# Kernel optimization log

Measured on AMD Instinct MI355X. Metric: run time of the kernel, lower is better.

## Reference

```python
import jax, jax.numpy as jnp
import numpy as np

B = 4          # clouds per batch
N_PER = 8192   # points per cloud
RATIO = 0.5
M = int(N_PER * RATIO)   # sampled centroids per cloud
R = 0.2        # radius
K = 64         # max_num_neighbors
C_IN = 64


def setup_inputs() -> dict:
    key = jax.random.key(0)
    k1, k2, k3, k4 = jax.random.split(key, 4)
    N = B * N_PER
    x = jax.random.normal(k1, (N, C_IN), dtype=jnp.float32)
    pos = jax.random.uniform(k2, (N, 3), dtype=jnp.float32)  # unit cube
    batch = jnp.repeat(jnp.arange(B, dtype=jnp.int32), N_PER)
    W1 = jax.random.normal(k3, (C_IN + 3, 64), dtype=jnp.float32) * (1.0 / np.sqrt(C_IN + 3))
    b1 = jnp.zeros((64,), dtype=jnp.float32)
    W2 = jax.random.normal(k4, (64, 128), dtype=jnp.float32) * (1.0 / np.sqrt(64))
    b2 = jnp.zeros((128,), dtype=jnp.float32)
    return {"x": x, "pos": pos, "batch": batch, "W1": W1, "b1": b1, "W2": W2, "b2": b2}


def _fps(posb):
    """Farthest point sampling, vectorized over clouds. posb: [B, n, 3] -> idx [B, M]."""
    d0 = jnp.sum((posb - posb[:, :1]) ** 2, axis=-1)  # dist^2 to seed point 0: [B, n]

    def step(dists, _):
        far = jnp.argmax(dists, axis=1)                              # [B]
        newp = jnp.take_along_axis(posb, far[:, None, None], axis=1)  # [B, 1, 3]
        d = jnp.sum((posb - newp) ** 2, axis=-1)                      # [B, n]
        return jnp.minimum(dists, d), far.astype(jnp.int32)

    _, rest = jax.lax.scan(step, d0, None, length=M - 1)  # rest: [M-1, B]
    return jnp.concatenate([jnp.zeros((B, 1), jnp.int32), rest.T], axis=1)  # [B, M]


def reference(x, pos, batch, W1, b1, W2, b2):
    posb = pos.reshape(B, N_PER, 3)
    xb = x.reshape(B, N_PER, C_IN)

    # --- fps ---
    idx = _fps(posb)                                         # [B, M]
    q = jnp.take_along_axis(posb, idx[:, :, None], axis=1)   # sampled centroids [B, M, 3]

    # --- radius query: K nearest neighbors within radius R (same cloud) ---
    d2 = jnp.sum((q[:, :, None, :] - posb[:, None, :, :]) ** 2, axis=-1)  # [B, M, n]
    neg = jnp.where(d2 <= R * R, -d2, -jnp.inf)
    vals, nbr = jax.lax.top_k(neg, K)                        # [B, M, K]
    valid = vals > -jnp.inf                                  # neighbor mask

    # --- PointNetConv: gather -> MLP -> masked max aggregation ---
    bidx = jnp.arange(B)[:, None, None]
    xj = xb[bidx, nbr]                                       # [B, M, K, C_IN]
    rel = posb[bidx, nbr] - q[:, :, None, :]                 # [B, M, K, 3]
    feat = jnp.concatenate([xj, rel], axis=-1)               # [B, M, K, C_IN+3]
    h = jax.nn.relu(feat @ W1 + b1)                          # [B, M, K, 64]
    h = jax.nn.relu(h @ W2 + b2)                             # [B, M, K, 128]
    h = jnp.where(valid[..., None], h, -jnp.inf)
    out = jnp.max(h, axis=2)                                 # [B, M, 128]; self-edge guarantees >=1 valid

    x_out = out.reshape(B * M, 128)
    pos_out = q.reshape(B * M, 3)
    batch_out = jnp.repeat(jnp.arange(B, dtype=batch.dtype), M)
    return x_out, pos_out, batch_out
```

## Files before the change

kernel.cpp:

```cpp
#include <hip/hip_runtime.h>
#include <stdint.h>

#define NPER 8192
#define NB 4
#define MPER 4096
#define MTOT (NB*MPER)
#define KNB 64
#define CIN 64
#define R2C 0.04f

#define POSOUT_OFF (MTOT*128)
#define BATCH_OFF  (MTOT*128 + MTOT*3)

#define SSTR 30720

typedef float v2f __attribute__((ext_vector_type(2)));

#define FPS_T 1024
#define PTS 8
#define NCELL 512

#define OFF_XS 0
#define OFF_YS (OFF_XS + NPER*4)
#define OFF_ZS (OFF_YS + NPER*4)
#define OFF_OS (OFF_ZS + NPER*4)
#define OFF_WIN (OFF_OS + NPER*2)
#define OFF_HIST (OFF_WIN + MPER*2)
#define OFF_SCAN (OFF_HIST + NCELL*4)
#define OFF_SLOT (OFF_SCAN + NCELL*4)
#define OFF_SID0 (OFF_SLOT + 24)
#define FPS_LDS  (OFF_SID0 + 8)

template<int CTRL>
__device__ __forceinline__ unsigned dppmax(unsigned v) {
  unsigned t = (unsigned)__builtin_amdgcn_update_dpp(
      0, (int)v, CTRL, 0xf, 0xf, true);
  return v > t ? v : t;
}
__device__ __forceinline__ unsigned wave_max_u32(unsigned v) {
  v = dppmax<0x111>(v);
  v = dppmax<0x112>(v);
  v = dppmax<0x114>(v);
  v = dppmax<0x118>(v);
  v = dppmax<0x142>(v);
  v = dppmax<0x143>(v);
  return (unsigned)__builtin_amdgcn_readlane((int)v, 63);
}

__global__ __launch_bounds__(1024) void k_fps(const float* __restrict__ pos,
                                              float* __restrict__ dout)
{
#pragma clang fp contract(off)
  extern __shared__ char smem[];
  float* Xs = (float*)(smem + OFF_XS);
  float* Ys = (float*)(smem + OFF_YS);
  float* Zs = (float*)(smem + OFF_ZS);
  unsigned short* Os = (unsigned short*)(smem + OFF_OS);
  unsigned short* winb = (unsigned short*)(smem + OFF_WIN);
  unsigned* hist = (unsigned*)(smem + OFF_HIST);
  unsigned* scanb = (unsigned*)(smem + OFF_SCAN);
  unsigned long long* slot3 = (unsigned long long*)(smem + OFF_SLOT);
  unsigned* sid0p = (unsigned*)(smem + OFF_SID0);

  const int b = blockIdx.x;
  const int tid = threadIdx.x;
  const float* pb = pos + (size_t)b * NPER * 3;
  float* qo = dout + POSOUT_OFF + (size_t)b * MPER * 3;
  float* scrb = dout + (size_t)b * SSTR;
  float* gSX = scrb; float* gSY = scrb + 8192; float* gSZ = scrb + 16384;
  unsigned* gSO = (unsigned*)(scrb + 24576);
  unsigned* gCS = (unsigned*)(scrb + 28672);

  if (tid < NCELL) hist[tid] = 0u;
  if (tid == 0) { slot3[0] = 0ull; slot3[1] = 0ull; slot3[2] = 0ull; }
  __syncthreads();

  float sxv[PTS], syv[PTS], szv[PTS];
  unsigned cellv[PTS];
#pragma unroll
  for (int k = 0; k < PTS; ++k) {
    int i = k * FPS_T + tid;
    sxv[k] = pb[i*3+0]; syv[k] = pb[i*3+1]; szv[k] = pb[i*3+2];
    unsigned ix = min(7u, (unsigned)(int)(sxv[k] * 8.0f));
    unsigned iy = min(7u, (unsigned)(int)(syv[k] * 8.0f));
    unsigned iz = min(7u, (unsigned)(int)(szv[k] * 8.0f));
    cellv[k] = (ix << 6) | (iy << 3) | iz;
    atomicAdd(&hist[cellv[k]], 1u);
  }
  __syncthreads();
  if (tid < NCELL) scanb[tid] = hist[tid];
  __syncthreads();
  for (int s = 1; s < NCELL; s <<= 1) {
    unsigned v = 0u;
    if (tid >= s && tid < NCELL) v = scanb[tid - s];
    __syncthreads();
    if (tid >= s && tid < NCELL) scanb[tid] += v;
    __syncthreads();
  }
  if (tid < NCELL) {
    hist[tid] = scanb[tid] - hist[tid];
    gCS[tid+1] = scanb[tid];
  }
  if (tid == 0) gCS[0] = 0u;
  __syncthreads();
#pragma unroll
  for (int k = 0; k < PTS; ++k) {
    unsigned dst = atomicAdd(&hist[cellv[k]], 1u);
    int orig = k * FPS_T + tid;
    Xs[dst] = sxv[k]; Ys[dst] = syv[k]; Zs[dst] = szv[k];
    Os[dst] = (unsigned short)orig;
    if (orig == 0) *sid0p = dst;
  }
  __syncthreads();
  for (int e = tid; e < NPER; e += FPS_T) {
    gSX[e] = Xs[e]; gSY[e] = Ys[e]; gSZ[e] = Zs[e];
  }
  for (int e = tid; e < NPER/2; e += FPS_T)
    gSO[e] = ((const unsigned*)Os)[e];
  v2f Xp[4], Yp[4], Zp[4], Dp[4];
  unsigned RK[PTS];
  float bxlo = 3.402823466e+38f, bylo = bxlo, bzlo = bxlo;
  float bxhi = -bxlo, byhi = bxhi, bzhi = bxhi;
#pragma unroll
  for (int k = 0; k < PTS; ++k) {
    int s = tid * PTS + k;
    float xx = Xs[s], yy = Ys[s], zz = Zs[s];
    Xp[k>>1][k&1] = xx; Yp[k>>1][k&1] = yy; Zp[k>>1][k&1] = zz;
    Dp[k>>1][k&1] = 3.402823466e+38f;
    unsigned orig = Os[s];
    RK[k] = ((unsigned)(NPER - 1 - orig) << 13) | (unsigned)s;
    bxlo = fminf(bxlo, xx); bxhi = fmaxf(bxhi, xx);
    bylo = fminf(bylo, yy); byhi = fmaxf(byhi, yy);
    bzlo = fminf(bzlo, zz); bzhi = fmaxf(bzhi, zz);
  }

  unsigned long long tkey = 0ull, wkey = 0ull;
  float lmax = 3.402823466e+38f;
  unsigned sidx = *sid0p;
  for (int m = 1; m < MPER; ++m) {
    const float cx = Xs[sidx], cy = Ys[sidx], cz = Zs[sidx];
    if (tid == 0) winb[m-1] = (unsigned short)sidx;
    if (tid == 1) slot3[(m+1) % 3] = 0ull;
    float ax = fmaxf(fmaxf(__fsub_rn(bxlo, cx), __fsub_rn(cx, bxhi)), 0.0f);
    float ay = fmaxf(fmaxf(__fsub_rn(bylo, cy), __fsub_rn(cy, byhi)), 0.0f);
    float az = fmaxf(fmaxf(__fsub_rn(bzlo, cz), __fsub_rn(cz, bzhi)), 0.0f);
    float lb = ax*ax + ay*ay + az*az;
    bool upd = (lb * 0.99988f) < lmax;
    if (__ballot(upd) != 0ull) {
      if (upd) {
        v2f cx2 = {cx, cx}, cy2 = {cy, cy}, cz2 = {cz, cz};
        v2f dnp[4];
        float bd = -1.0f;
#pragma unroll
        for (int p = 0; p < 4; ++p) {
          v2f dx = Xp[p] - cx2;
          v2f dy = Yp[p] - cy2;
          v2f dz = Zp[p] - cz2;
          v2f s = (dx*dx + dy*dy) + dz*dz;
          v2f dn;
          dn.x = fminf(Dp[p].x, s.x);
          dn.y = fminf(Dp[p].y, s.y);
          Dp[p] = dn; dnp[p] = dn;
          bd = fmaxf(bd, fmaxf(dn.x, dn.y));
        }
        unsigned brk = 0u;
#pragma unroll
        for (int p = 0; p < 4; ++p) {
          brk = (dnp[p].x == bd) ? max(brk, RK[2*p])   : brk;
          brk = (dnp[p].y == bd) ? max(brk, RK[2*p+1]) : brk;
        }
        tkey = ((unsigned long long)__float_as_uint(bd) << 26) | brk;
        lmax = bd;
      }
      unsigned hi = (unsigned)(tkey >> 26);
      unsigned M = wave_max_u32(hi);
      unsigned rk = (unsigned)tkey & 0x3FFFFFFu;
      unsigned long long msk = __ballot(hi == M);
      unsigned lo;
      if (__popcll(msk) == 1) {
        int ln = (int)__builtin_ctzll(msk);
        lo = (unsigned)__builtin_amdgcn_readlane((int)rk, ln);
      } else {
        lo = wave_max_u32((hi == M) ? rk : 0u);
      }
      wkey = ((unsigned long long)M << 26) | lo;
    }
    if ((tid & 63) == 0) atomicMax(&slot3[m % 3], wkey);
    __syncthreads();
    sidx = (unsigned)(slot3[m % 3] & 0x1FFFull);
  }
  if (tid == 0) winb[MPER-1] = (unsigned short)sidx;
  __syncthreads();
  for (int e = tid; e < MPER; e += FPS_T) {
    unsigned s = winb[e];
    qo[e*3+0] = Xs[s]; qo[e*3+1] = Ys[s]; qo[e*3+2] = Zs[s];
  }
}

#define SCAP 512
__global__ __launch_bounds__(256) void k_radius(const float* __restrict__ pos,
    float* __restrict__ dout, unsigned short* __restrict__ nbr,
    int* __restrict__ cnt)
{
  __shared__ unsigned candH[4][SCAP];
  __shared__ unsigned candL[4][SCAP];
  const int wid = threadIdx.x >> 6, lane = threadIdx.x & 63;
  const int m = blockIdx.x * 4 + wid;
  const int b = m >> 12;
  const float* scrb = dout + (size_t)b * SSTR;
  const float* SX = scrb;
  const float* SY = scrb + 8192;
  const float* SZ = scrb + 16384;
  const unsigned short* SO = (const unsigned short*)(scrb + 24576);
  const unsigned* CS = (const unsigned*)(scrb + 28672);
  const float* q = dout + POSOUT_OFF + (size_t)m * 3;
  const float qx = q[0], qy = q[1], qz = q[2];
  const int ixc = min(7, (int)(qx * 8.0f));
  const int iyc = min(7, (int)(qy * 8.0f));
  const int izc = min(7, (int)(qz * 8.0f));
  const int izlo = max(izc-2, 0), izhi = min(izc+2, 7);
  unsigned s0v = 0u, s1v = 0u;
  {
    int ix = ixc + lane / 5 - 2;
    int iy = iyc + lane % 5 - 2;
    if (lane < 25 && ix >= 0 && ix < 8 && iy >= 0 && iy < 8) {
      int cb = (ix << 6) | (iy << 3);
      s0v = CS[cb + izlo];
      s1v = CS[cb + izhi + 1];
    }
  }
  unsigned cw = 0;
  for (int seg = 0; seg < 25; ++seg) {
    unsigned s0 = (unsigned)__builtin_amdgcn_readlane((int)s0v, seg);
    unsigned s1 = (unsigned)__builtin_amdgcn_readlane((int)s1v, seg);
    for (unsigned i0 = s0; i0 < s1; i0 += 64) {
      unsigned i = i0 + (unsigned)lane;
      float dx = __fsub_rn(qx, SX[i]);
      float dy = __fsub_rn(qy, SY[i]);
      float dz = __fsub_rn(qz, SZ[i]);
      float d2 = __fadd_rn(__fadd_rn(__fmul_rn(dx,dx), __fmul_rn(dy,dy)),
                           __fmul_rn(dz,dz));
      bool in = (i < s1) && (d2 <= R2C);
      unsigned long long mk = __ballot(in);
      unsigned pre = (unsigned)__popcll(mk & ((1ull << lane) - 1ull));
      if (in) {
        unsigned slot = cw + pre;
        if (slot < SCAP) {
          candH[wid][slot] = __float_as_uint(d2);
          candL[wid][slot] = (unsigned)SO[i];
        }
      }
      cw += (unsigned)__popcll(mk);
    }
  }
  if (cw > SCAP) cw = SCAP;
  for (int s = (int)cw + lane; s < SCAP; s += 64) {
    candH[wid][s] = 0xFFFFFFFFu; candL[wid][s] = 0xFFFFFFFFu;
  }
  __syncthreads();
  for (int k = 2; k <= SCAP; k <<= 1) {
    for (int j = k >> 1; j > 0; j >>= 1) {
#pragma unroll
      for (int s = 0; s < SCAP/128; ++s) {
        int t = lane + (s << 6);
        int e = ((t & ~(j-1)) << 1) | (t & (j-1));
        int p = e | j;
        unsigned aH = candH[wid][e], aL = candL[wid][e];
        unsigned cH = candH[wid][p], cL = candL[wid][p];
        bool agt = (aH > cH) || (aH == cH && aL > cL);
        bool asc = ((e & k) == 0);
        bool sw = asc ? agt : !agt && (aH != cH || aL != cL);
        if (sw) {
          candH[wid][e] = cH; candL[wid][e] = cL;
          candH[wid][p] = aH; candL[wid][p] = aL;
        }
      }
      __syncthreads();
    }
  }
  int kk = (int)cw; if (kk > KNB) kk = KNB;
  nbr[(size_t)m*KNB + lane] =
    (lane < kk) ? (unsigned short)(candL[wid][lane] & 0xFFFFu)
                : (unsigned short)0;
  if (lane == 0) {
    cnt[m] = kk;
    dout[BATCH_OFF + m] = (float)b;
  }
}

__global__ __launch_bounds__(128) void k_conv(
    const float* __restrict__ x, const float* __restrict__ pos,
    const float* __restrict__ W1, const float* __restrict__ b1,
    const float* __restrict__ W2, const float* __restrict__ b2,
    const unsigned short* __restrict__ nbr, const int* __restrict__ cntp,
    float* __restrict__ dout)
{
  __shared__ __align__(16) float bufA[68*68];
  __shared__ __align__(16) float bufB[68*68];
  __shared__ unsigned short nbr_s[64];
  __shared__ float qv[3];
  __shared__ int cnt_s;
  const int t = threadIdx.x;
  const int m = blockIdx.x;
  const int b = m >> 12;
  if (t < 64) nbr_s[t] = nbr[(size_t)m*KNB + t];
  else if (t == 64) cnt_s = cntp[m];
  else if (t >= 65 && t < 68) qv[t-65] = dout[POSOUT_OFF + (size_t)m*3 + (t-65)];
  for (int e = t; e < 67*64; e += 128) {
    int ch = e >> 6, h = e & 63;
    bufB[ch*68 + h] = W1[e];
  }
  __syncthreads();
  {
    const int ch = t & 63, jj = t >> 6;
    const size_t xb = (size_t)b * NPER * CIN;
    for (int j0 = 0; j0 < 64; j0 += 2) {
      int j = j0 + jj;
      int r = nbr_s[j];
      bufA[ch*68 + j] = x[xb + (size_t)r*CIN + ch];
    }
  }
  {
    const size_t pbb = (size_t)b * NPER * 3;
    for (int e = t; e < 192; e += 128) {
      int j = e & 63, d = e >> 6;
      int r = nbr_s[j];
      bufA[(64+d)*68 + j] = pos[pbb + (size_t)r*3 + d] - qv[d];
    }
  }
  __syncthreads();

  const int jg = t & 7, hg = t >> 3;
  const int j0 = jg << 3;
  const int h0 = hg << 2;
  v2f accp[4][4];
#pragma unroll
  for (int hh = 0; hh < 4; ++hh)
#pragma unroll
    for (int jp = 0; jp < 4; ++jp) accp[hh][jp] = (v2f){0.0f, 0.0f};
  for (int ch = 0; ch < 67; ++ch) {
    const float4 fa = *(const float4*)&bufA[ch*68 + j0];
    const float4 fb = *(const float4*)&bufA[ch*68 + j0 + 4];
    const float4 w  = *(const float4*)&bufB[ch*68 + h0];
    const v2f fj[4] = {{fa.x, fa.y}, {fa.z, fa.w}, {fb.x, fb.y}, {fb.z, fb.w}};
    const float ws4[4] = {w.x, w.y, w.z, w.w};
#pragma unroll
    for (int hh = 0; hh < 4; ++hh) {
      const v2f wv2 = {ws4[hh], ws4[hh]};
#pragma unroll
      for (int jp = 0; jp < 4; ++jp)
        accp[hh][jp] += wv2 * fj[jp];
    }
  }
  __syncthreads();
  {
    const float4 bb = *(const float4*)&b1[h0];
    const float bv[4] = {bb.x, bb.y, bb.z, bb.w};
#pragma unroll
    for (int hh = 0; hh < 4; ++hh) {
      float4 o0, o1;
      o0.x = fmaxf(accp[hh][0].x + bv[hh], 0.0f);
      o0.y = fmaxf(accp[hh][0].y + bv[hh], 0.0f);
      o0.z = fmaxf(accp[hh][1].x + bv[hh], 0.0f);
      o0.w = fmaxf(accp[hh][1].y + bv[hh], 0.0f);
      o1.x = fmaxf(accp[hh][2].x + bv[hh], 0.0f);
      o1.y = fmaxf(accp[hh][2].y + bv[hh], 0.0f);
      o1.z = fmaxf(accp[hh][3].x + bv[hh], 0.0f);
      o1.w = fmaxf(accp[hh][3].y + bv[hh], 0.0f);
      *(float4*)&bufA[(h0+hh)*68 + j0] = o0;
      *(float4*)&bufA[(h0+hh)*68 + j0 + 4] = o1;
    }
  }
  const int c0 = hg << 3;
  v2f acc2p[8][4];
#pragma unroll
  for (int c = 0; c < 8; ++c)
#pragma unroll
    for (int jp = 0; jp < 4; ++jp) acc2p[c][jp] = (v2f){0.0f, 0.0f};
  for (int hc = 0; hc < 64; hc += 16) {
    __syncthreads();
    for (int e = t; e < 16*128; e += 128) {
      int hh = e >> 7, c = e & 127;
      bufB[hh*136 + c] = W2[(size_t)(hc+hh)*128 + c];
    }
    __syncthreads();
#pragma unroll
    for (int h = 0; h < 16; ++h) {
      const float4 ja = *(const float4*)&bufA[(hc+h)*68 + j0];
      const float4 jb = *(const float4*)&bufA[(hc+h)*68 + j0 + 4];
      const float4 wa = *(const float4*)&bufB[h*136 + c0];
      const float4 wb = *(const float4*)&bufB[h*136 + c0 + 4];
      const v2f hj[4] = {{ja.x, ja.y}, {ja.z, ja.w}, {jb.x, jb.y}, {jb.z, jb.w}};
      const float wv[8] = {wa.x, wa.y, wa.z, wa.w, wb.x, wb.y, wb.z, wb.w};
#pragma unroll
      for (int c = 0; c < 8; ++c) {
        const v2f w2 = {wv[c], wv[c]};
#pragma unroll
        for (int jp = 0; jp < 4; ++jp)
          acc2p[c][jp] += w2 * hj[jp];
      }
    }
  }
  const int cntv = cnt_s;
  const float4 b2a = *(const float4*)&b2[c0];
  const float4 b2b = *(const float4*)&b2[c0 + 4];
  const float bv2[8] = {b2a.x, b2a.y, b2a.z, b2a.w, b2b.x, b2b.y, b2b.z, b2b.w};
  float best[8];
#pragma unroll
  for (int c = 0; c < 8; ++c) {
    float v = -3.402823466e+38f;
#pragma unroll
    for (int jp = 0; jp < 4; ++jp) {
      float h0v = fmaxf(acc2p[c][jp].x + bv2[c], 0.0f);
      float h1v = fmaxf(acc2p[c][jp].y + bv2[c], 0.0f);
      v = (j0 + 2*jp     < cntv) ? fmaxf(v, h0v) : v;
      v = (j0 + 2*jp + 1 < cntv) ? fmaxf(v, h1v) : v;
    }
    best[c] = v;
  }
#pragma unroll
  for (int off = 1; off < 8; off <<= 1)
#pragma unroll
    for (int c = 0; c < 8; ++c)
      best[c] = fmaxf(best[c], __shfl_xor(best[c], off));
  if (jg == 0) {
    float4 o0 = {best[0], best[1], best[2], best[3]};
    float4 o1 = {best[4], best[5], best[6], best[7]};
    *(float4*)&dout[(size_t)m*128 + c0] = o0;
    *(float4*)&dout[(size_t)m*128 + c0 + 4] = o1;
  }
}

extern "C" void kernel_launch(void* const* d_in, const int* in_sizes, int n_in,
                              void* d_out, int out_size, void* d_ws, size_t ws_size,
                              hipStream_t stream) {
  const float* x   = (const float*)d_in[0];
  const float* pos = (const float*)d_in[1];
  const float* W1  = (const float*)d_in[3];
  const float* b1  = (const float*)d_in[4];
  const float* W2  = (const float*)d_in[5];
  const float* b2  = (const float*)d_in[6];
  float* dout = (float*)d_out;
  unsigned short* nbr = (unsigned short*)d_ws;
  int* cnt = (int*)((char*)d_ws + (size_t)MTOT*KNB*2);

  hipLaunchKernelGGL(k_fps,    dim3(NB),     dim3(FPS_T), FPS_LDS, stream, pos, dout);
  hipLaunchKernelGGL(k_radius, dim3(MTOT/4), dim3(256),   0, stream, pos, dout, nbr, cnt);
  hipLaunchKernelGGL(k_conv,   dim3(MTOT),   dim3(128),   0, stream,
                     x, pos, W1, b1, W2, b2, nbr, cnt, dout);
}
```

Baseline: 3.121 ms.

## Precompute x@W1 per point, pack FPS positions as float4, split wave-max slots

After: 3.294 ms. 1.06x slower.

```diff
diff --git a/kernel.cpp b/kernel.cpp
--- a/kernel.cpp
+++ b/kernel.cpp
@@ -12,6 +12,9 @@
 #define POSOUT_OFF (MTOT*128)
 #define BATCH_OFF  (MTOT*128 + MTOT*3)
 
+#define PRE_OFF 2162688ull
+#define PRE_BYTES 8388608ull
+
 #define SSTR 30720
 
 typedef float v2f __attribute__((ext_vector_type(2)));
@@ -20,16 +23,11 @@
 #define PTS 8
 #define NCELL 512
 
-#define OFF_XS 0
-#define OFF_YS (OFF_XS + NPER*4)
-#define OFF_ZS (OFF_YS + NPER*4)
-#define OFF_OS (OFF_ZS + NPER*4)
-#define OFF_WIN (OFF_OS + NPER*2)
-#define OFF_HIST (OFF_WIN + MPER*2)
-#define OFF_SCAN (OFF_HIST + NCELL*4)
-#define OFF_SLOT (OFF_SCAN + NCELL*4)
-#define OFF_SID0 (OFF_SLOT + 24)
-#define FPS_LDS  (OFF_SID0 + 8)
+#define OFF_XYZ4 0
+#define OFF_WIN  (OFF_XYZ4 + NPER*16)
+#define OFF_SLOT (OFF_WIN + MPER*2)
+#define OFF_SID0 (OFF_SLOT + 96)
+#define FPS_LDS  (OFF_SID0 + 16)
 
 template<int CTRL>
 __device__ __forceinline__ unsigned dppmax(unsigned v) {
@@ -52,18 +50,16 @@
 {
 #pragma clang fp contract(off)
   extern __shared__ char smem[];
-  float* Xs = (float*)(smem + OFF_XS);
-  float* Ys = (float*)(smem + OFF_YS);
-  float* Zs = (float*)(smem + OFF_ZS);
-  unsigned short* Os = (unsigned short*)(smem + OFF_OS);
+  float4* X4 = (float4*)(smem + OFF_XYZ4);
   unsigned short* winb = (unsigned short*)(smem + OFF_WIN);
-  unsigned* hist = (unsigned*)(smem + OFF_HIST);
-  unsigned* scanb = (unsigned*)(smem + OFF_SCAN);
-  unsigned long long* slot3 = (unsigned long long*)(smem + OFF_SLOT);
+  unsigned* hist = (unsigned*)(smem + OFF_WIN);
+  unsigned* scanb = (unsigned*)(smem + OFF_WIN + 2048);
+  unsigned long long* slot12 = (unsigned long long*)(smem + OFF_SLOT);
   unsigned* sid0p = (unsigned*)(smem + OFF_SID0);
 
   const int b = blockIdx.x;
   const int tid = threadIdx.x;
+  const int wv = tid >> 6;
   const float* pb = pos + (size_t)b * NPER * 3;
   float* qo = dout + POSOUT_OFF + (size_t)b * MPER * 3;
   float* scrb = dout + (size_t)b * SSTR;
@@ -72,7 +68,7 @@
   unsigned* gCS = (unsigned*)(scrb + 28672);
 
   if (tid < NCELL) hist[tid] = 0u;
-  if (tid == 0) { slot3[0] = 0ull; slot3[1] = 0ull; slot3[2] = 0ull; }
+  if (tid < 12) slot12[tid] = 0ull;
   __syncthreads();
 
   float sxv[PTS], syv[PTS], szv[PTS];
@@ -107,16 +103,22 @@
   for (int k = 0; k < PTS; ++k) {
     unsigned dst = atomicAdd(&hist[cellv[k]], 1u);
     int orig = k * FPS_T + tid;
-    Xs[dst] = sxv[k]; Ys[dst] = syv[k]; Zs[dst] = szv[k];
-    Os[dst] = (unsigned short)orig;
+    float4 v;
+    v.x = sxv[k]; v.y = syv[k]; v.z = szv[k];
+    v.w = __uint_as_float((unsigned)orig);
+    X4[dst] = v;
     if (orig == 0) *sid0p = dst;
   }
   __syncthreads();
   for (int e = tid; e < NPER; e += FPS_T) {
-    gSX[e] = Xs[e]; gSY[e] = Ys[e]; gSZ[e] = Zs[e];
-  }
-  for (int e = tid; e < NPER/2; e += FPS_T)
-    gSO[e] = ((const unsigned*)Os)[e];
+    float4 v = X4[e];
+    gSX[e] = v.x; gSY[e] = v.y; gSZ[e] = v.z;
+  }
+  for (int e = tid; e < NPER/2; e += FPS_T) {
+    unsigned o0 = __float_as_uint(X4[2*e].w) & 0xFFFFu;
+    unsigned o1 = __float_as_uint(X4[2*e+1].w) & 0xFFFFu;
+    gSO[e] = o0 | (o1 << 16);
+  }
   v2f Xp[4], Yp[4], Zp[4], Dp[4];
   unsigned RK[PTS];
   float bxlo = 3.402823466e+38f, bylo = bxlo, bzlo = bxlo;
@@ -124,23 +126,25 @@
 #pragma unroll
   for (int k = 0; k < PTS; ++k) {
     int s = tid * PTS + k;
-    float xx = Xs[s], yy = Ys[s], zz = Zs[s];
-    Xp[k>>1][k&1] = xx; Yp[k>>1][k&1] = yy; Zp[k>>1][k&1] = zz;
+    float4 v = X4[s];
+    Xp[k>>1][k&1] = v.x; Yp[k>>1][k&1] = v.y; Zp[k>>1][k&1] = v.z;
     Dp[k>>1][k&1] = 3.402823466e+38f;
-    unsigned orig = Os[s];
+    unsigned orig = __float_as_uint(v.w);
     RK[k] = ((unsigned)(NPER - 1 - orig) << 13) | (unsigned)s;
-    bxlo = fminf(bxlo, xx); bxhi = fmaxf(bxhi, xx);
-    bylo = fminf(bylo, yy); byhi = fmaxf(byhi, yy);
-    bzlo = fminf(bzlo, zz); bzhi = fmaxf(bzhi, zz);
+    bxlo = fminf(bxlo, v.x); bxhi = fmaxf(bxhi, v.x);
+    bylo = fminf(bylo, v.y); byhi = fmaxf(byhi, v.y);
+    bzlo = fminf(bzlo, v.z); bzhi = fmaxf(bzhi, v.z);
   }
 
   unsigned long long tkey = 0ull, wkey = 0ull;
   float lmax = 3.402823466e+38f;
   unsigned sidx = *sid0p;
   for (int m = 1; m < MPER; ++m) {
-    const float cx = Xs[sidx], cy = Ys[sidx], cz = Zs[sidx];
+    const float4 c4 = X4[sidx];
+    const float cx = c4.x, cy = c4.y, cz = c4.z;
     if (tid == 0) winb[m-1] = (unsigned short)sidx;
-    if (tid == 1) slot3[(m+1) % 3] = 0ull;
+    if (tid >= 4 && tid < 8)
+      slot12[((m+1) % 3)*4 + (tid-4)] = 0ull;
     float ax = fmaxf(fmaxf(__fsub_rn(bxlo, cx), __fsub_rn(cx, bxhi)), 0.0f);
     float ay = fmaxf(fmaxf(__fsub_rn(bylo, cy), __fsub_rn(cy, byhi)), 0.0f);
     float az = fmaxf(fmaxf(__fsub_rn(bzlo, cz), __fsub_rn(cz, bzhi)), 0.0f);
@@ -185,15 +189,21 @@
       }
       wkey = ((unsigned long long)M << 26) | lo;
     }
-    if ((tid & 63) == 0) atomicMax(&slot3[m % 3], wkey);
+    const int ph = (m % 3) * 4;
+    if ((tid & 63) == 0) atomicMax(&slot12[ph + (wv & 3)], wkey);
     __syncthreads();
-    sidx = (unsigned)(slot3[m % 3] & 0x1FFFull);
+    unsigned long long k0 = slot12[ph+0], k1 = slot12[ph+1];
+    unsigned long long k2 = slot12[ph+2], k3 = slot12[ph+3];
+    k0 = (k1 > k0) ? k1 : k0;
+    k2 = (k3 > k2) ? k3 : k2;
+    k0 = (k2 > k0) ? k2 : k0;
+    sidx = (unsigned)(k0 & 0x1FFFull);
   }
   if (tid == 0) winb[MPER-1] = (unsigned short)sidx;
   __syncthreads();
   for (int e = tid; e < MPER; e += FPS_T) {
-    unsigned s = winb[e];
-    qo[e*3+0] = Xs[s]; qo[e*3+1] = Ys[s]; qo[e*3+2] = Zs[s];
+    float4 v = X4[winb[e]];
+    qo[e*3+0] = v.x; qo[e*3+1] = v.y; qo[e*3+2] = v.z;
   }
 }
 
@@ -288,6 +298,152 @@
   }
 }
 
+__global__ __launch_bounds__(256) void k_pre(const float* __restrict__ x,
+    const float* __restrict__ W1, float* __restrict__ hp)
+{
+  __shared__ float Ws[64*64];
+  __shared__ float Xs[64][65];
+  const int t = threadIdx.x;
+  const int row0 = blockIdx.x * 64;
+  for (int e = t; e < 64*64; e += 256) Ws[e] = W1[e];
+  for (int e = t; e < 64*64; e += 256) {
+    int r = e >> 6, ch = e & 63;
+    Xs[r][ch] = x[(size_t)(row0 + r) * 64 + ch];
+  }
+  __syncthreads();
+  const int rg = t >> 4, cg = t & 15;
+  const int r0 = rg << 2, c0 = cg << 2;
+  float acc[4][4];
+#pragma unroll
+  for (int r = 0; r < 4; ++r)
+#pragma unroll
+    for (int c = 0; c < 4; ++c) acc[r][c] = 0.0f;
+  for (int k = 0; k < 64; ++k) {
+    const float4 w = *(const float4*)&Ws[(k << 6) + c0];
+    const float xr[4] = {Xs[r0][k], Xs[r0+1][k], Xs[r0+2][k], Xs[r0+3][k]};
+    const float wc[4] = {w.x, w.y, w.z, w.w};
+#pragma unroll
+    for (int r = 0; r < 4; ++r)
+#pragma unroll
+      for (int c = 0; c < 4; ++c)
+        acc[r][c] = fmaf(xr[r], wc[c], acc[r][c]);
+  }
+#pragma unroll
+  for (int r = 0; r < 4; ++r) {
+    float4 o = {acc[r][0], acc[r][1], acc[r][2], acc[r][3]};
+    *(float4*)&hp[(size_t)(row0 + r0 + r) * 64 + c0] = o;
+  }
+}
+
+__global__ __launch_bounds__(128) void k_conv2(
+    const float* __restrict__ hp, const float* __restrict__ pos,
+    const float* __restrict__ W1, const float* __restrict__ b1,
+    const float* __restrict__ W2, const float* __restrict__ b2,
+    const unsigned short* __restrict__ nbr, const int* __restrict__ cntp,
+    float* __restrict__ dout)
+{
+  __shared__ __align__(16) float bufA[68*68];
+  __shared__ __align__(16) float bufB[16*136];
+  __shared__ float w1p[3*64];
+  __shared__ unsigned short nbr_s[64];
+  __shared__ float qv[3];
+  __shared__ int cnt_s;
+  const int t = threadIdx.x;
+  const int m = blockIdx.x;
+  const int b = m >> 12;
+  if (t < 64) nbr_s[t] = nbr[(size_t)m*KNB + t];
+  else if (t == 64) cnt_s = cntp[m];
+  else if (t >= 65 && t < 68) qv[t-65] = dout[POSOUT_OFF + (size_t)m*3 + (t-65)];
+  for (int e = t; e < 192; e += 128) w1p[e] = W1[64*64 + e];
+  __syncthreads();
+  {
+    const int h = t & 63, jj = t >> 6;
+    const size_t hb = (size_t)b * NPER * 64;
+    for (int j0 = 0; j0 < 64; j0 += 2) {
+      int j = j0 + jj;
+      int r = nbr_s[j];
+      bufA[h*68 + j] = hp[hb + (size_t)r*64 + h];
+    }
+  }
+  {
+    const size_t pbb = (size_t)b * NPER * 3;
+    for (int e = t; e < 192; e += 128) {
+      int j = e & 63, d = e >> 6;
+      int r = nbr_s[j];
+      bufA[(64+d)*68 + j] = pos[pbb + (size_t)r*3 + d] - qv[d];
+    }
+  }
+  __syncthreads();
+  for (int e = t; e < 64*64; e += 128) {
+    int h = e >> 6, j = e & 63;
+    float v = bufA[h*68 + j];
+    v = fmaf(bufA[64*68 + j], w1p[h],       v);
+    v = fmaf(bufA[65*68 + j], w1p[64 + h],  v);
+    v = fmaf(bufA[66*68 + j], w1p[128 + h], v);
+    bufA[h*68 + j] = fmaxf(v + b1[h], 0.0f);
+  }
+  const int jg = t & 7, hg = t >> 3;
+  const int j0 = jg << 3;
+  const int c0 = hg << 3;
+  v2f acc2p[8][4];
+#pragma unroll
+  for (int c = 0; c < 8; ++c)
+#pragma unroll
+    for (int jp = 0; jp < 4; ++jp) acc2p[c][jp] = (v2f){0.0f, 0.0f};
+  for (int hc = 0; hc < 64; hc += 16) {
+    __syncthreads();
+    for (int e = t; e < 16*128; e += 128) {
+      int hh = e >> 7, c = e & 127;
+      bufB[hh*136 + c] = W2[(size_t)(hc+hh)*128 + c];
+    }
+    __syncthreads();
+#pragma unroll
+    for (int h = 0; h < 16; ++h) {
+      const float4 ja = *(const float4*)&bufA[(hc+h)*68 + j0];
+      const float4 jb = *(const float4*)&bufA[(hc+h)*68 + j0 + 4];
+      const float4 wa = *(const float4*)&bufB[h*136 + c0];
+      const float4 wb = *(const float4*)&bufB[h*136 + c0 + 4];
+      const v2f hj[4] = {{ja.x, ja.y}, {ja.z, ja.w}, {jb.x, jb.y}, {jb.z, jb.w}};
+      const float wv[8] = {wa.x, wa.y, wa.z, wa.w, wb.x, wb.y, wb.z, wb.w};
+#pragma unroll
+      for (int c = 0; c < 8; ++c) {
+        const v2f w2 = {wv[c], wv[c]};
+#pragma unroll
+        for (int jp = 0; jp < 4; ++jp)
+          acc2p[c][jp] += w2 * hj[jp];
+      }
+    }
+  }
+  const int cntv = cnt_s;
+  const float4 b2a = *(const float4*)&b2[c0];
+  const float4 b2b = *(const float4*)&b2[c0 + 4];
+  const float bv2[8] = {b2a.x, b2a.y, b2a.z, b2a.w, b2b.x, b2b.y, b2b.z, b2b.w};
+  float best[8];
+#pragma unroll
+  for (int c = 0; c < 8; ++c) {
+    float v = -3.402823466e+38f;
+#pragma unroll
+    for (int jp = 0; jp < 4; ++jp) {
+      float h0v = fmaxf(acc2p[c][jp].x + bv2[c], 0.0f);
+      float h1v = fmaxf(acc2p[c][jp].y + bv2[c], 0.0f);
+      v = (j0 + 2*jp     < cntv) ? fmaxf(v, h0v) : v;
+      v = (j0 + 2*jp + 1 < cntv) ? fmaxf(v, h1v) : v;
+    }
+    best[c] = v;
+  }
+#pragma unroll
+  for (int off = 1; off < 8; off <<= 1)
+#pragma unroll
+    for (int c = 0; c < 8; ++c)
+      best[c] = fmaxf(best[c], __shfl_xor(best[c], off));
+  if (jg == 0) {
+    float4 o0 = {best[0], best[1], best[2], best[3]};
+    float4 o1 = {best[4], best[5], best[6], best[7]};
+    *(float4*)&dout[(size_t)m*128 + c0] = o0;
+    *(float4*)&dout[(size_t)m*128 + c0 + 4] = o1;
+  }
+}
+
 __global__ __launch_bounds__(128) void k_conv(
     const float* __restrict__ x, const float* __restrict__ pos,
     const float* __restrict__ W1, const float* __restrict__ b1,
@@ -329,7 +485,6 @@
     }
   }
   __syncthreads();
-
   const int jg = t & 7, hg = t >> 3;
   const int j0 = jg << 3;
   const int h0 = hg << 2;
@@ -443,9 +598,17 @@
   float* dout = (float*)d_out;
   unsigned short* nbr = (unsigned short*)d_ws;
   int* cnt = (int*)((char*)d_ws + (size_t)MTOT*KNB*2);
+  float* hp = (float*)((char*)d_ws + PRE_OFF);
+  const bool use_pre = (ws_size >= PRE_OFF + PRE_BYTES);
 
   hipLaunchKernelGGL(k_fps,    dim3(NB),     dim3(FPS_T), FPS_LDS, stream, pos, dout);
   hipLaunchKernelGGL(k_radius, dim3(MTOT/4), dim3(256),   0, stream, pos, dout, nbr, cnt);
-  hipLaunchKernelGGL(k_conv,   dim3(MTOT),   dim3(128),   0, stream,
-                     x, pos, W1, b1, W2, b2, nbr, cnt, dout);
-}
+  if (use_pre) {
+    hipLaunchKernelGGL(k_pre,   dim3(NB*NPER/64), dim3(256), 0, stream, x, W1, hp);
+    hipLaunchKernelGGL(k_conv2, dim3(MTOT),       dim3(128), 0, stream,
+                       hp, pos, W1, b1, W2, b2, nbr, cnt, dout);
+  } else {
+    hipLaunchKernelGGL(k_conv,  dim3(MTOT),       dim3(128), 0, stream,
+                       x, pos, W1, b1, W2, b2, nbr, cnt, dout);
+  }
+}
```
